# Kernel optimization log

Hardware: AMD Instinct MI355X
Metric: run time of the kernel (lower is better)

The kernel has to match this reference:

```python
import jax, jax.numpy as jnp
import numpy as np

B, D, E, H1, H2 = 64, 2048, 64, 512, 256
EPS = 1e-5


def setup_inputs() -> dict:
    key = jax.random.key(0)
    ks = jax.random.split(key, 8)
    s = lambda k, shape, scale: jax.random.normal(k, shape, dtype=jnp.float32) * scale
    return {
        "sparse_representation": s(ks[0], (B, D), 1.0),
        "emb": s(ks[1], (D, E), 1.0),
        "W1": s(ks[2], (D + E, H1), (D + E) ** -0.5),
        "b1": s(ks[3], (H1,), 0.02),
        "g1": jnp.ones((H1,), jnp.float32),
        "beta1": jnp.zeros((H1,), jnp.float32),
        "m1": jnp.zeros((H1,), jnp.float32),
        "v1": jnp.ones((H1,), jnp.float32),
        "W2": s(ks[4], (H1, H2), H1 ** -0.5),
        "b2": s(ks[5], (H2,), 0.02),
        "g2": jnp.ones((H2,), jnp.float32),
        "beta2": jnp.zeros((H2,), jnp.float32),
        "m2": jnp.zeros((H2,), jnp.float32),
        "v2": jnp.ones((H2,), jnp.float32),
        "W3": s(ks[6], (H2, 1), H2 ** -0.5),
        "b3": s(ks[7], (1,), 0.02),
    }


def _bn_relu(x, g, beta, m, v):
    # eval-mode BatchNorm1d followed by ReLU
    return jax.nn.relu((x - m) * jax.lax.rsqrt(v + EPS) * g + beta)


def reference(sparse_representation, emb, W1, b1, g1, beta1, m1, v1,
              W2, b2, g2, beta2, m2, v2, W3, b3):
    rep = sparse_representation  # (B, D)
    W1d, W1e = W1[:D], W1[D:]    # (D, H1), (E, H1)
    # Fused predict_all: for each k, masked input zeros column k, so
    # Linear(masked_k) = rep @ W1d - rep[:, k] * W1d[k]
    base = rep @ W1d + b1                       # (B, H1)
    emb_h = emb @ W1e                           # (D, H1) per-index embedding contribution
    h1 = base[:, None, :] + emb_h[None, :, :] - rep[:, :, None] * W1d[None, :, :]  # (B, D, H1)
    h1 = _bn_relu(h1, g1, beta1, m1, v1)
    h2 = jnp.einsum("bkh,ho->bko", h1, W2) + b2  # (B, D, H2)
    h2 = _bn_relu(h2, g2, beta2, m2, v2)
    out = jnp.einsum("bkh,h->bk", h2, W3[:, 0]) + b3[0]  # (B, D)
    return out
```

## Files before the change

kernel.cpp:

```cpp
#include <hip/hip_runtime.h>

#define EPS 1e-5f

typedef __attribute__((ext_vector_type(8))) short short8;
typedef __attribute__((ext_vector_type(4))) float f32x4;

__device__ __forceinline__ float bflo(unsigned u) { return __uint_as_float(u << 16); }
__device__ __forceinline__ float bfhi(unsigned u) { return __uint_as_float(u & 0xffff0000u); }
__device__ __forceinline__ unsigned short f2bf(float f) {
  unsigned u = __float_as_uint(f);
  u = u + 0x7FFFu + ((u >> 16) & 1u);
  return (unsigned short)(u >> 16);
}
__device__ __forceinline__ unsigned pack2(float a, float b) {
  return (unsigned)f2bf(a) | ((unsigned)f2bf(b) << 16);
}

__global__ __launch_bounds__(256) void prep2(
    const float* __restrict__ emb, const float* __restrict__ W1,
    const float* __restrict__ g1, const float* __restrict__ v1,
    const float* __restrict__ b1, const float* __restrict__ m1,
    const float* __restrict__ beta1,
    const float* __restrict__ W2,
    const float* __restrict__ g2, const float* __restrict__ v2,
    const float* __restrict__ b2, const float* __restrict__ m2,
    const float* __restrict__ beta2,
    unsigned* __restrict__ Q, unsigned* __restrict__ R,
    unsigned short* __restrict__ W2t,
    float* __restrict__ t2, float* __restrict__ c2, float* __restrict__ Pf) {
  __shared__ float smem[256];
  const int x = blockIdx.x, t = threadIdx.x;
  if (x < 512) {
    const int k0 = x * 4;
    smem[t] = emb[x * 256 + t];
    __syncthreads();
    const int h = t * 2;
    const float a0 = g1[h] * rsqrtf(v1[h] + EPS);
    const float a1 = g1[h + 1] * rsqrtf(v1[h + 1] + EPS);
    const float pb0 = a0 * (b1[h] - m1[h]) + beta1[h];
    const float pb1 = a1 * (b1[h + 1] - m1[h + 1]) + beta1[h + 1];
    const float* We = W1 + 2048 * 512;
    float acc0[4], acc1[4];
    #pragma unroll
    for (int k = 0; k < 4; ++k) { acc0[k] = 0.f; acc1[k] = 0.f; }
    #pragma unroll 4
    for (int e = 0; e < 64; ++e) {
      float2 wv = *(const float2*)(We + e * 512 + h);
      #pragma unroll
      for (int k = 0; k < 4; ++k) {
        float ev = smem[k * 64 + e];
        acc0[k] = fmaf(ev, wv.x, acc0[k]);
        acc1[k] = fmaf(ev, wv.y, acc1[k]);
      }
    }
    #pragma unroll
    for (int k = 0; k < 4; ++k) {
      Q[(k0 + k) * 256 + t] = pack2(a0 * acc0[k] + pb0, a1 * acc1[k] + pb1);
      float2 wv = *(const float2*)(W1 + (size_t)(k0 + k) * 512 + h);
      R[(k0 + k) * 256 + t] = pack2(a0 * wv.x, a1 * wv.y);
    }
  } else if (x < 576) {
    const int h0 = (x - 512) * 8;
    const int o = t;
    unsigned d[4];
    #pragma unroll
    for (int i = 0; i < 4; ++i) {
      float v0 = W2[(h0 + 2 * i) * 256 + o];
      float v1_ = W2[(h0 + 2 * i + 1) * 256 + o];
      d[i] = pack2(v0, v1_);
    }
    *(uint4*)(W2t + o * 512 + h0) = make_uint4(d[0], d[1], d[2], d[3]);
  } else {
    float tv = g2[t] * rsqrtf(v2[t] + EPS);
    t2[t] = tv;
    c2[t] = tv * (b2[t] - m2[t]) + beta2[t];
    f32x4 z = (f32x4){0.f, 0.f, 0.f, 0.f};
    #pragma unroll 8
    for (int j = 0; j < 32; ++j)
      *(f32x4*)(Pf + ((size_t)(j * 256 + t)) * 4) = z;
  }
}

__global__ __launch_bounds__(256) void p_gemm(
    const float* __restrict__ rep, const unsigned* __restrict__ R,
    float* __restrict__ Pf) {
  __shared__ float red[4][512];
  const int b = blockIdx.x >> 3, ksl = blockIdx.x & 7;
  const int t = threadIdx.x, lane = t & 63, kq = t >> 6;
  const int kbase = ksl * 256 + kq * 64;
  const unsigned* Rp = R + (size_t)kbase * 256 + lane * 4;
  const float* rp = rep + b * 2048 + kbase;
  float acc[8];
  #pragma unroll
  for (int i = 0; i < 8; ++i) acc[i] = 0.f;
  #pragma unroll 8
  for (int k = 0; k < 64; ++k) {
    uint4 rv = *(const uint4*)(Rp + (size_t)k * 256);
    float rk = rp[k];
    acc[0] = fmaf(rk, bflo(rv.x), acc[0]); acc[1] = fmaf(rk, bfhi(rv.x), acc[1]);
    acc[2] = fmaf(rk, bflo(rv.y), acc[2]); acc[3] = fmaf(rk, bfhi(rv.y), acc[3]);
    acc[4] = fmaf(rk, bflo(rv.z), acc[4]); acc[5] = fmaf(rk, bfhi(rv.z), acc[5]);
    acc[6] = fmaf(rk, bflo(rv.w), acc[6]); acc[7] = fmaf(rk, bfhi(rv.w), acc[7]);
  }
  *(f32x4*)(&red[kq][lane * 8])     = (f32x4){acc[0], acc[1], acc[2], acc[3]};
  *(f32x4*)(&red[kq][lane * 8 + 4]) = (f32x4){acc[4], acc[5], acc[6], acc[7]};
  __syncthreads();
  {
    const int h = t * 2;
    float s0 = red[0][h] + red[1][h] + red[2][h] + red[3][h];
    float s1 = red[0][h + 1] + red[1][h + 1] + red[2][h + 1] + red[3][h + 1];
    atomicAdd(&Pf[b * 512 + h], s0);
    atomicAdd(&Pf[b * 512 + h + 1], s1);
  }
}

__global__ __launch_bounds__(256) void pf2p(const float* __restrict__ Pf,
                                            unsigned* __restrict__ P) {
  const int i = blockIdx.x * 256 + threadIdx.x;
  float2 v = *(const float2*)(Pf + 2 * i);
  P[i] = pack2(v.x, v.y);
}

__global__ __launch_bounds__(256, 2) void fused_main(
    const float* __restrict__ rep,
    const unsigned* __restrict__ P,
    const unsigned* __restrict__ Q,
    const unsigned* __restrict__ Rm,
    const unsigned short* __restrict__ W2t,
    const float* __restrict__ t2, const float* __restrict__ c2,
    const float* __restrict__ W3, const float* __restrict__ b3,
    float* __restrict__ out) {
  __shared__ unsigned short A_lds[2][8192];
  __shared__ float partial[4][128];

  const int t = threadIdx.x;
  const int w = t >> 6;
  const int ln = t & 15;
  const int lq = (t >> 4) & 3;
  const int ks_id = w & 1;
  const int hi_id = w >> 1;
  const int k0 = blockIdx.x * 2;

  float rb[4];
  #pragma unroll
  for (int p = 0; p < 4; ++p) {
    int r = (p * 2 + hi_id) * 16 + ln;
    rb[p] = rep[(r & 63) * 2048 + k0 + (r >> 6)];
  }

  f32x4 acc[8][4];
  #pragma unroll
  for (int mi = 0; mi < 8; ++mi)
    #pragma unroll
    for (int nj = 0; nj < 4; ++nj) acc[mi][nj] = (f32x4){0.f, 0.f, 0.f, 0.f};

  uint4 s_p[4], s_q[4], s_r[4];

  auto genLoad = [&](int c) {
    const int cb2 = (c * 64 + ks_id * 32 + lq * 8) >> 1;
    #pragma unroll
    for (int p = 0; p < 4; ++p) {
      const int r = (p * 2 + hi_id) * 16 + ln;
      const int bb = r & 63;
      const int kg = k0 + (r >> 6);
      s_p[p] = *(const uint4*)(P + (bb << 8) + cb2);
      s_q[p] = *(const uint4*)(Q + (kg << 8) + cb2);
      s_r[p] = *(const uint4*)(Rm + (kg << 8) + cb2);
    }
  };
  auto genStore = [&](unsigned short* buf) {
    #pragma unroll
    for (int p = 0; p < 4; ++p) {
      const float rp_ = rb[p];
      unsigned d[4];
      float z0, z1;
      z0 = fmaf(-rp_, bflo(s_r[p].x), bflo(s_p[p].x) + bflo(s_q[p].x));
      z1 = fmaf(-rp_, bfhi(s_r[p].x), bfhi(s_p[p].x) + bfhi(s_q[p].x));
      d[0] = pack2(fmaxf(z0, 0.f), fmaxf(z1, 0.f));
      z0 = fmaf(-rp_, bflo(s_r[p].y), bflo(s_p[p].y) + bflo(s_q[p].y));
      z1 = fmaf(-rp_, bfhi(s_r[p].y), bfhi(s_p[p].y) + bfhi(s_q[p].y));
      d[1] = pack2(fmaxf(z0, 0.f), fmaxf(z1, 0.f));
      z0 = fmaf(-rp_, bflo(s_r[p].z), bflo(s_p[p].z) + bflo(s_q[p].z));
      z1 = fmaf(-rp_, bfhi(s_r[p].z), bfhi(s_p[p].z) + bfhi(s_q[p].z));
      d[2] = pack2(fmaxf(z0, 0.f), fmaxf(z1, 0.f));
      z0 = fmaf(-rp_, bflo(s_r[p].w), bflo(s_p[p].w) + bflo(s_q[p].w));
      z1 = fmaf(-rp_, bfhi(s_r[p].w), bfhi(s_p[p].w) + bfhi(s_q[p].w));
      d[3] = pack2(fmaxf(z0, 0.f), fmaxf(z1, 0.f));
      *(uint4*)(&buf[(size_t)(p * 256 + t) * 8]) = make_uint4(d[0], d[1], d[2], d[3]);
    }
  };
  auto mfma_chunk = [&](const unsigned short* buf, int c) {
    #pragma unroll
    for (int ks = 0; ks < 2; ++ks) {
      short8 afr[8];
      #pragma unroll
      for (int mi = 0; mi < 8; ++mi)
        afr[mi] = *(const short8*)(buf + (size_t)((((mi * 2 + ks) * 4 + lq) * 16 + ln) * 8));
      short8 bfr[4];
      #pragma unroll
      for (int nj = 0; nj < 4; ++nj)
        bfr[nj] = *(const short8*)(W2t + (size_t)(w * 64 + nj * 16 + ln) * 512 + c * 64 + ks * 32 + lq * 8);
      #pragma unroll
      for (int mi = 0; mi < 8; ++mi)
        #pragma unroll
        for (int nj = 0; nj < 4; ++nj)
          acc[mi][nj] = __builtin_amdgcn_mfma_f32_16x16x32_bf16(afr[mi], bfr[nj], acc[mi][nj], 0, 0, 0);
    }
  };

  genLoad(0);
  genStore(A_lds[0]);
  genLoad(1);

  for (int c = 0; c < 8; ++c) {
    __syncthreads();
    if (c < 7) genStore(A_lds[(c + 1) & 1]);
    if (c < 6) genLoad(c + 2);
    mfma_chunk(A_lds[c & 1], c);
  }

  float t2v[4], c2v[4], w3v[4];
  #pragma unroll
  for (int nj = 0; nj < 4; ++nj) {
    int o = w * 64 + nj * 16 + ln;
    t2v[nj] = t2[o];
    c2v[nj] = c2[o];
    w3v[nj] = W3[o];
  }
  #pragma unroll
  for (int mi = 0; mi < 8; ++mi) {
    float s[4] = {0.f, 0.f, 0.f, 0.f};
    #pragma unroll
    for (int nj = 0; nj < 4; ++nj)
      #pragma unroll
      for (int r = 0; r < 4; ++r) {
        float u = fmaf(t2v[nj], acc[mi][nj][r], c2v[nj]);
        u = fmaxf(u, 0.f);
        s[r] = fmaf(u, w3v[nj], s[r]);
      }
    #pragma unroll
    for (int r = 0; r < 4; ++r) {
      #pragma unroll
      for (int m = 1; m < 16; m <<= 1) s[r] += __shfl_xor(s[r], m, 64);
    }
    if (ln == 0) {
      #pragma unroll
      for (int r = 0; r < 4; ++r) partial[w][mi * 16 + lq * 4 + r] = s[r];
    }
  }
  __syncthreads();
  if (t < 128) {
    out[(t & 63) * 2048 + k0 + (t >> 6)] =
        partial[0][t] + partial[1][t] + partial[2][t] + partial[3][t] + b3[0];
  }
}

extern "C" void kernel_launch(void* const* d_in, const int* in_sizes, int n_in,
                              void* d_out, int out_size, void* d_ws, size_t ws_size,
                              hipStream_t stream) {
  const float* rep   = (const float*)d_in[0];
  const float* emb   = (const float*)d_in[1];
  const float* W1    = (const float*)d_in[2];
  const float* b1    = (const float*)d_in[3];
  const float* g1    = (const float*)d_in[4];
  const float* beta1 = (const float*)d_in[5];
  const float* m1    = (const float*)d_in[6];
  const float* v1    = (const float*)d_in[7];
  const float* W2    = (const float*)d_in[8];
  const float* b2    = (const float*)d_in[9];
  const float* g2    = (const float*)d_in[10];
  const float* beta2 = (const float*)d_in[11];
  const float* m2    = (const float*)d_in[12];
  const float* v2    = (const float*)d_in[13];
  const float* W3    = (const float*)d_in[14];
  const float* b3    = (const float*)d_in[15];
  float* out = (float*)d_out;
  char* ws = (char*)d_ws;

  float* Pf            = (float*)(ws + 0);
  unsigned* P          = (unsigned*)(ws + 131072);
  unsigned* Q          = (unsigned*)(ws + 196608);
  unsigned* R          = (unsigned*)(ws + 2293760);
  unsigned short* W2t  = (unsigned short*)(ws + 4390912);
  float* t2            = (float*)(ws + 4653056);
  float* c2            = (float*)(ws + 4654080);

  prep2<<<577, 256, 0, stream>>>(emb, W1, g1, v1, b1, m1, beta1, W2, g2, v2,
                                 b2, m2, beta2, Q, R, W2t, t2, c2, Pf);
  p_gemm<<<512, 256, 0, stream>>>(rep, R, Pf);
  pf2p<<<64, 256, 0, stream>>>(Pf, P);
  fused_main<<<1024, 256, 0, stream>>>(rep, P, Q, R, W2t, t2, c2, W3, b3, out);
}
```

Before: 171.4 us.

## Build MFMA A-fragments directly in registers, dropping LDS staging and barriers

Each wave now generates its own bf16 A fragments in registers from P, Q and Rm instead of cooperatively writing h1 tiles to a double-buffered LDS array and reading them back after __syncthreads. This removes the LDS traffic and the per-chunk block barriers. In exchange each wave redundantly recomputes the same A tile, so the elementwise work and global/L2 loads of P rows are duplicated across the four waves, and register pressure rises from two sets of prefetch buffers.

Result: slower. 357.9 us (+108.9%).

```diff
diff --git a/kernel.cpp b/kernel.cpp
--- a/kernel.cpp
+++ b/kernel.cpp
@@ -130,23 +130,18 @@
     const float* __restrict__ t2, const float* __restrict__ c2,
     const float* __restrict__ W3, const float* __restrict__ b3,
     float* __restrict__ out) {
-  __shared__ unsigned short A_lds[2][8192];
   __shared__ float partial[4][128];
 
   const int t = threadIdx.x;
   const int w = t >> 6;
   const int ln = t & 15;
   const int lq = (t >> 4) & 3;
-  const int ks_id = w & 1;
-  const int hi_id = w >> 1;
   const int k0 = blockIdx.x * 2;
 
-  float rb[4];
-  #pragma unroll
-  for (int p = 0; p < 4; ++p) {
-    int r = (p * 2 + hi_id) * 16 + ln;
-    rb[p] = rep[(r & 63) * 2048 + k0 + (r >> 6)];
-  }
+  float rb[8];
+  #pragma unroll
+  for (int mi = 0; mi < 8; ++mi)
+    rb[mi] = rep[((mi & 3) * 16 + ln) * 2048 + k0 + (mi >> 2)];
 
   f32x4 acc[8][4];
   #pragma unroll
@@ -154,69 +149,75 @@
     #pragma unroll
     for (int nj = 0; nj < 4; ++nj) acc[mi][nj] = (f32x4){0.f, 0.f, 0.f, 0.f};
 
-  uint4 s_p[4], s_q[4], s_r[4];
-
-  auto genLoad = [&](int c) {
-    const int cb2 = (c * 64 + ks_id * 32 + lq * 8) >> 1;
-    #pragma unroll
-    for (int p = 0; p < 4; ++p) {
-      const int r = (p * 2 + hi_id) * 16 + ln;
-      const int bb = r & 63;
-      const int kg = k0 + (r >> 6);
-      s_p[p] = *(const uint4*)(P + (bb << 8) + cb2);
-      s_q[p] = *(const uint4*)(Q + (kg << 8) + cb2);
-      s_r[p] = *(const uint4*)(Rm + (kg << 8) + cb2);
+  uint4 p0[4], q0[2], r0[2];
+  uint4 p1[4], q1[2], r1[2];
+
+  auto loadS = [&](int c, int ks, uint4 (&sp)[4], uint4 (&sq)[2], uint4 (&sr)[2]) {
+    const int cb2 = c * 32 + ks * 16 + lq * 4;
+    #pragma unroll
+    for (int j = 0; j < 4; ++j)
+      sp[j] = *(const uint4*)(P + ((j * 16 + ln) << 8) + cb2);
+    #pragma unroll
+    for (int i = 0; i < 2; ++i) {
+      sq[i] = *(const uint4*)(Q + ((size_t)(k0 + i) << 8) + cb2);
+      sr[i] = *(const uint4*)(Rm + ((size_t)(k0 + i) << 8) + cb2);
     }
   };
-  auto genStore = [&](unsigned short* buf) {
-    #pragma unroll
-    for (int p = 0; p < 4; ++p) {
-      const float rp_ = rb[p];
-      unsigned d[4];
-      float z0, z1;
-      z0 = fmaf(-rp_, bflo(s_r[p].x), bflo(s_p[p].x) + bflo(s_q[p].x));
-      z1 = fmaf(-rp_, bfhi(s_r[p].x), bfhi(s_p[p].x) + bfhi(s_q[p].x));
-      d[0] = pack2(fmaxf(z0, 0.f), fmaxf(z1, 0.f));
-      z0 = fmaf(-rp_, bflo(s_r[p].y), bflo(s_p[p].y) + bflo(s_q[p].y));
-      z1 = fmaf(-rp_, bfhi(s_r[p].y), bfhi(s_p[p].y) + bfhi(s_q[p].y));
-      d[1] = pack2(fmaxf(z0, 0.f), fmaxf(z1, 0.f));
-      z0 = fmaf(-rp_, bflo(s_r[p].z), bflo(s_p[p].z) + bflo(s_q[p].z));
-      z1 = fmaf(-rp_, bfhi(s_r[p].z), bfhi(s_p[p].z) + bfhi(s_q[p].z));
-      d[2] = pack2(fmaxf(z0, 0.f), fmaxf(z1, 0.f));
-      z0 = fmaf(-rp_, bflo(s_r[p].w), bflo(s_p[p].w) + bflo(s_q[p].w));
-      z1 = fmaf(-rp_, bfhi(s_r[p].w), bfhi(s_p[p].w) + bfhi(s_q[p].w));
-      d[3] = pack2(fmaxf(z0, 0.f), fmaxf(z1, 0.f));
-      *(uint4*)(&buf[(size_t)(p * 256 + t) * 8]) = make_uint4(d[0], d[1], d[2], d[3]);
-    }
+
+  auto packfrag = [&](const uint4& pv, const uint4& qv, const uint4& rv,
+                      float rp_) -> short8 {
+    unsigned d0, d1, d2, d3;
+    float z0, z1;
+    z0 = fmaf(-rp_, bflo(rv.x), bflo(pv.x) + bflo(qv.x));
+    z1 = fmaf(-rp_, bfhi(rv.x), bfhi(pv.x) + bfhi(qv.x));
+    d0 = pack2(fmaxf(z0, 0.f), fmaxf(z1, 0.f));
+    z0 = fmaf(-rp_, bflo(rv.y), bflo(pv.y) + bflo(qv.y));
+    z1 = fmaf(-rp_, bfhi(rv.y), bfhi(pv.y) + bfhi(qv.y));
+    d1 = pack2(fmaxf(z0, 0.f), fmaxf(z1, 0.f));
+    z0 = fmaf(-rp_, bflo(rv.z), bflo(pv.z) + bflo(qv.z));
+    z1 = fmaf(-rp_, bfhi(rv.z), bfhi(pv.z) + bfhi(qv.z));
+    d2 = pack2(fmaxf(z0, 0.f), fmaxf(z1, 0.f));
+    z0 = fmaf(-rp_, bflo(rv.w), bflo(pv.w) + bflo(qv.w));
+    z1 = fmaf(-rp_, bfhi(rv.w), bfhi(pv.w) + bfhi(qv.w));
+    d3 = pack2(fmaxf(z0, 0.f), fmaxf(z1, 0.f));
+    uint4 dd = make_uint4(d0, d1, d2, d3);
+    return *(short8*)&dd;
   };
-  auto mfma_chunk = [&](const unsigned short* buf, int c) {
-    #pragma unroll
-    for (int ks = 0; ks < 2; ++ks) {
-      short8 afr[8];
-      #pragma unroll
-      for (int mi = 0; mi < 8; ++mi)
-        afr[mi] = *(const short8*)(buf + (size_t)((((mi * 2 + ks) * 4 + lq) * 16 + ln) * 8));
-      short8 bfr[4];
+
+  auto half = [&](int c, int ks, uint4 (&sp)[4], uint4 (&sq)[2], uint4 (&sr)[2],
+                  bool reload) {
+    short8 bfr[4];
+    #pragma unroll
+    for (int nj = 0; nj < 4; ++nj)
+      bfr[nj] = *(const short8*)(W2t + (size_t)(w * 64 + nj * 16 + ln) * 512 +
+                                 c * 64 + ks * 32 + lq * 8);
+    short8 afr[4];
+    #pragma unroll
+    for (int mi = 0; mi < 4; ++mi)
+      afr[mi] = packfrag(sp[mi], sq[0], sr[0], rb[mi]);
+    #pragma unroll
+    for (int mi = 0; mi < 4; ++mi)
       #pragma unroll
       for (int nj = 0; nj < 4; ++nj)
-        bfr[nj] = *(const short8*)(W2t + (size_t)(w * 64 + nj * 16 + ln) * 512 + c * 64 + ks * 32 + lq * 8);
-      #pragma unroll
-      for (int mi = 0; mi < 8; ++mi)
-        #pragma unroll
-        for (int nj = 0; nj < 4; ++nj)
-          acc[mi][nj] = __builtin_amdgcn_mfma_f32_16x16x32_bf16(afr[mi], bfr[nj], acc[mi][nj], 0, 0, 0);
-    }
+        acc[mi][nj] = __builtin_amdgcn_mfma_f32_16x16x32_bf16(afr[mi], bfr[nj], acc[mi][nj], 0, 0, 0);
+    #pragma unroll
+    for (int mi = 0; mi < 4; ++mi)
+      afr[mi] = packfrag(sp[mi], sq[1], sr[1], rb[4 + mi]);
+    if (reload) loadS(c + 1, ks, sp, sq, sr);
+    #pragma unroll
+    for (int mi = 0; mi < 4; ++mi)
+      #pragma unroll
+      for (int nj = 0; nj < 4; ++nj)
+        acc[4 + mi][nj] = __builtin_amdgcn_mfma_f32_16x16x32_bf16(afr[mi], bfr[nj], acc[4 + mi][nj], 0, 0, 0);
   };
 
-  genLoad(0);
-  genStore(A_lds[0]);
-  genLoad(1);
-
+  loadS(0, 0, p0, q0, r0);
+  loadS(0, 1, p1, q1, r1);
+
+  #pragma unroll 1
   for (int c = 0; c < 8; ++c) {
-    __syncthreads();
-    if (c < 7) genStore(A_lds[(c + 1) & 1]);
-    if (c < 6) genLoad(c + 2);
-    mfma_chunk(A_lds[c & 1], c);
+    half(c, 0, p0, q0, r0, c < 7);
+    half(c, 1, p1, q1, r1, c < 7);
   }
 
   float t2v[4], c2v[4], w3v[4];
```
